# Kernel optimization log

Measured on AMD Instinct MI355X. Metric: run time of the kernel, lower is better.

Reference implementation:

```python
import jax, jax.numpy as jnp
import numpy as np

HEAD = 4
EPS = 1e-12


def _l2norm(x, axis):
    # torch F.normalize: x / max(||x||_2, eps)
    return x / jnp.maximum(jnp.linalg.norm(x, axis=axis, keepdims=True), EPS)


def setup_inputs() -> dict:
    key = jax.random.key(0)
    ks = jax.random.split(key, 12)
    n, t, c, h, w = 2, 7, 96, 96, 96
    inp = {
        "curr_feat": jax.random.normal(ks[0], (n, c, h, w), jnp.float32),
        "index_feat_set_s1": jax.random.normal(ks[1], (n, t, c, h, w), jnp.float32),
        "anchor_feat": jax.random.normal(ks[2], (n, c, h, w), jnp.float32),
        "sparse_feat_set_s1": jax.random.normal(ks[3], (n, t, c, h, w), jnp.float32),
        "sparse_feat_set_s2": jax.random.normal(ks[4], (n, t, c, h, w), jnp.float32),
        "sparse_feat_set_s3": jax.random.normal(ks[5], (n, t, c, h, w), jnp.float32),
        # absolute pixel coordinates (x,y interleaved per frame), mostly in-bounds
        # with a little overshoot to exercise zeros padding of grid_sample
        "location_feat": jax.random.uniform(ks[6], (n, t * 2, h, w), jnp.float32, minval=-2.0, maxval=float(w) + 1.0),
        "proj_w": 0.02 * jax.random.normal(ks[7], (c, c), jnp.float32),
        "proj_b": jnp.zeros((c,), jnp.float32),
        "fusion_w": 0.02 * jax.random.normal(ks[8], (c, 3 * c), jnp.float32),
        "fusion_b": jnp.zeros((c,), jnp.float32),
    }
    return inp


def reference(curr_feat, index_feat_set_s1, anchor_feat, sparse_feat_set_s1,
              sparse_feat_set_s2, sparse_feat_set_s3, location_feat,
              proj_w, proj_b, fusion_w, fusion_b):
    n, c, h, w = anchor_feat.shape
    t = sparse_feat_set_s1.shape[1]
    hd = c // HEAD
    hw = h * w

    # ---- flow-guided nearest grid_sample (align_corners=True, zeros pad) ----
    loc = location_feat.reshape(n, t, 2, h, w)  # (n,t,2,h,w): [x, y] pixel coords
    gx = 2.0 * loc[:, :, 0] / max(w - 1, 1) - 1.0
    gy = 2.0 * loc[:, :, 1] / max(h - 1, 1) - 1.0
    ix = jnp.round((gx + 1.0) * 0.5 * (w - 1))  # nearest (round-half-even, as torch)
    iy = jnp.round((gy + 1.0) * 0.5 * (h - 1))
    valid = (ix >= 0) & (ix <= w - 1) & (iy >= 0) & (iy <= h - 1)
    lin = (jnp.clip(iy, 0, h - 1).astype(jnp.int32) * w
           + jnp.clip(ix, 0, w - 1).astype(jnp.int32)).reshape(n, t, 1, hw)
    vmask = valid.reshape(n, t, 1, hw)

    def sample(f):  # f: (n,t,c,h,w) -> gathered (n,t,c,hw)
        g = jnp.take_along_axis(f.reshape(n, t, c, hw), lin, axis=3)
        return jnp.where(vmask, g, 0.0)

    samp1 = sample(sparse_feat_set_s1)
    samp2 = sample(sparse_feat_set_s2)
    samp3 = sample(sparse_feat_set_s3)
    sampi = sample(index_feat_set_s1)

    # ---- per-pixel multi-head max-correlation over t frames ----
    # queries: normalize over full channel dim c BEFORE splitting into heads
    q = _l2norm(curr_feat.reshape(n, c, hw).transpose(0, 2, 1), -1).reshape(n, hw, HEAD, hd)
    k = _l2norm(sampi.transpose(0, 3, 1, 2), -1).reshape(n, hw, t, HEAD, hd)
    scores = jnp.einsum('npthd,nphd->npht', k, q)  # scale == 1.0 in mode='max'
    corr_soft = jnp.max(scores, axis=3)     # (n,hw,head)
    corr_index = jnp.argmax(scores, axis=3)  # (n,hw,head), first-max like torch

    soft_img = jnp.broadcast_to(corr_soft[..., None], (n, hw, HEAD, hd)) \
                  .reshape(n, h, w, c).transpose(0, 3, 1, 2)  # (n,c,h,w)
    idx = jnp.broadcast_to(corr_index[..., None], (n, hw, HEAD, hd)) \
             .reshape(n, hw, c).transpose(0, 2, 1)[:, None]  # (n,1,c,hw)

    def pick(samp):  # select winning frame per (channel-group, pixel)
        return jnp.take_along_axis(samp, idx, axis=1)[:, 0].reshape(n, c, h, w)

    cat = jnp.concatenate([pick(samp1), pick(samp2), pick(samp3)], axis=1)  # (n,3c,h,w)
    out = jnp.einsum('ndhw,cd->nchw', cat, fusion_w) + fusion_b[None, :, None, None]
    out = out * soft_img
    out = jnp.einsum('nchw,dc->ndhw', out, proj_w) + proj_b[None, :, None, None]
    return out + anchor_feat
```

## Files before the change

### kernel.cpp

```cpp
#include <hip/hip_runtime.h>
#include <hip/hip_bf16.h>

#define N_    2
#define T_    7
#define C_    96
#define H_    96
#define W_    96
#define HW_   9216
#define HEAD_ 4
#define HD_   24
#define C3_   288
#define P_    16
#define QP_   100
#define CATP_ 292
#define NBLK_ (N_ * (HW_ / P_))
#define PLANES_ 14
#define CHUNK_  64
#define NCHUNK_ 144

typedef unsigned int u32;

__device__ __forceinline__ float bits2f(u32 b) {
    union { u32 u; float f; } x; x.u = b; return x.f;
}

__device__ __forceinline__ unsigned short f2bf(float f) {
    union { __hip_bfloat16 h; unsigned short s; } u;
    u.h = __float2bfloat16(f);
    return u.s;
}

template<bool BF16>
__device__ __forceinline__ float ld1(const void* p, int i) {
    if constexpr (BF16) return bits2f(((u32)((const unsigned short*)p)[i]) << 16);
    else                return ((const float*)p)[i];
}

template<bool BF16>
__device__ __forceinline__ void ld4w(const void* p, int i, float w[4]) {
    if constexpr (BF16) {
        const uint2 u = ((const uint2*)p)[i >> 2];
        w[0] = bits2f(u.x << 16);
        w[1] = bits2f(u.x & 0xFFFF0000u);
        w[2] = bits2f(u.y << 16);
        w[3] = bits2f(u.y & 0xFFFF0000u);
    } else {
        const float4 v = *((const float4*)((const float*)p + i));
        w[0] = v.x; w[1] = v.y; w[2] = v.z; w[3] = v.w;
    }
}

template<bool BF16>
__device__ __forceinline__ void st4w(void* p, int i, const float v[4]) {
    if constexpr (BF16) {
        uint2 w;
        w.x = (u32)f2bf(v[0]) | ((u32)f2bf(v[1]) << 16);
        w.y = (u32)f2bf(v[2]) | ((u32)f2bf(v[3]) << 16);
        ((uint2*)p)[i >> 2] = w;
    } else {
        *((float4*)((float*)p + i)) = make_float4(v[0], v[1], v[2], v[3]);
    }
}

__device__ __forceinline__ bool block_detect_bf16(const u32* __restrict__ w,
                                                  int tid, int* s_flag) {
    if (tid < 64) {
        u32 x = w[tid];
        u32 f = x & 0x7FFFu;
        int inwin = (f >= 0x3A00u) && (f <= 0x4200u);
        unsigned long long m = __ballot(inwin);
        if (tid == 0) *s_flag = (__popcll(m) >= 40) ? 1 : 0;
    }
    __syncthreads();
    return *s_flag != 0;
}

template<bool BF16>
__device__ __forceinline__ void transp_body(const void* __restrict__ src,
                                            void* __restrict__ dst,
                                            int bx, int tid, char* tileraw) {
    const int pl = bx / NCHUNK_;
    const int x0 = (bx - pl * NCHUNK_) * CHUNK_;
    if constexpr (BF16) {
        unsigned short (*tile)[CHUNK_ + 2] = (unsigned short (*)[CHUNK_ + 2])tileraw;
        const unsigned short* s = (const unsigned short*)src;
        unsigned short* d = (unsigned short*)dst;
        for (int i = tid; i < C_ * (CHUNK_ / 4); i += 256) {
            int ch = i >> 4, xq = i & 15;
            const ushort4 v = *((const ushort4*)(s + (pl * C_ + ch) * HW_ + x0 + 4 * xq));
            tile[ch][4 * xq + 0] = v.x; tile[ch][4 * xq + 1] = v.y;
            tile[ch][4 * xq + 2] = v.z; tile[ch][4 * xq + 3] = v.w;
        }
        __syncthreads();
        for (int i = tid; i < CHUNK_ * (C_ / 4); i += 256) {
            int p = i / 24, cq = i - p * 24;
            ushort4 v;
            v.x = tile[4 * cq + 0][p]; v.y = tile[4 * cq + 1][p];
            v.z = tile[4 * cq + 2][p]; v.w = tile[4 * cq + 3][p];
            *((ushort4*)(d + (pl * HW_ + x0 + p) * C_ + 4 * cq)) = v;
        }
    } else {
        float (*tile)[CHUNK_ + 1] = (float (*)[CHUNK_ + 1])tileraw;
        const float* s = (const float*)src;
        float* d = (float*)dst;
        for (int i = tid; i < C_ * (CHUNK_ / 4); i += 256) {
            int ch = i >> 4, xq = i & 15;
            const float4 v = *((const float4*)(s + (pl * C_ + ch) * HW_ + x0 + 4 * xq));
            tile[ch][4 * xq + 0] = v.x; tile[ch][4 * xq + 1] = v.y;
            tile[ch][4 * xq + 2] = v.z; tile[ch][4 * xq + 3] = v.w;
        }
        __syncthreads();
        for (int i = tid; i < CHUNK_ * (C_ / 4); i += 256) {
            int p = i / 24, cq = i - p * 24;
            float4 v;
            v.x = tile[4 * cq + 0][p]; v.y = tile[4 * cq + 1][p];
            v.z = tile[4 * cq + 2][p]; v.w = tile[4 * cq + 3][p];
            *((float4*)(d + (pl * HW_ + x0 + p) * C_ + 4 * cq)) = v;
        }
    }
}

__global__ __launch_bounds__(256) void transp_kernel(
    const void* __restrict__ idxf, void* __restrict__ dst,
    const u32* __restrict__ detect_src)
{
    __shared__ __align__(16) char tileraw[C_ * (CHUNK_ + 1) * 4];
    __shared__ int s_flag;
    const int tid = threadIdx.x;
    const bool bf = block_detect_bf16(detect_src, tid, &s_flag);
    if (bf) transp_body<true >(idxf, dst, blockIdx.x, tid, tileraw);
    else    transp_body<false>(idxf, dst, blockIdx.x, tid, tileraw);
}

template<bool BF16, int MODE>
__device__ __forceinline__ void traj_body(
    const void* __restrict__ curr, const void* __restrict__ idxf,
    const void* __restrict__ anchor, const void* __restrict__ s1,
    const void* __restrict__ s2, const void* __restrict__ s3,
    const void* __restrict__ loc, const void* __restrict__ pw,
    const void* __restrict__ pb, const void* __restrict__ fw,
    const void* __restrict__ fb, void* __restrict__ outp,
    const void* __restrict__ kT,
    float* s_u, float (*s_mid)[QP_], int (*s_lin)[P_], float (*s_red)[8],
    float (*s_best)[HEAD_], int (*s_bidx)[HEAD_], float* s_inv)
{
#define S_Q(pp, ch)  s_u[(pp) * QP_ + (ch)]
#define S_K(pp, ch)  s_u[P_ * QP_ + (pp) * QP_ + (ch)]
#define S_CAT(pp, d) s_u[(pp) * CATP_ + (d)]

    const int tid = threadIdx.x;
    const int b  = blockIdx.x;
    const int nn = b / (HW_ / P_);
    const int p0 = (b - nn * (HW_ / P_)) * P_;

    if (tid < T_ * P_) {
        int t = tid / P_, pp = tid - t * P_;
        int p = p0 + pp;
        float x = ld1<BF16>(loc, (nn * 2 * T_ + 2 * t    ) * HW_ + p);
        float y = ld1<BF16>(loc, (nn * 2 * T_ + 2 * t + 1) * HW_ + p);
        float gx = 2.0f * x / 95.0f - 1.0f;
        float gy = 2.0f * y / 95.0f - 1.0f;
        float fx = (gx + 1.0f) * 0.5f * 95.0f;
        float fy = (gy + 1.0f) * 0.5f * 95.0f;
        float ix = rintf(fx), iy = rintf(fy);
        bool v = (ix >= 0.0f) && (ix <= 95.0f) && (iy >= 0.0f) && (iy <= 95.0f);
        s_lin[t][pp] = v ? ((int)iy * W_ + (int)ix) : -1;
    }
    if (tid >= 128 && tid < 128 + P_ * HEAD_) {
        int q = tid - 128;
        s_best[q >> 2][q & 3] = -3.0e38f; s_bidx[q >> 2][q & 3] = 0;
    }

    for (int i = tid; i < C_ * (P_ / 4); i += 256) {
        int ch = i >> 2, pq = i & 3;
        float w[4];
        ld4w<BF16>(curr, (nn * C_ + ch) * HW_ + p0 + 4 * pq, w);
        S_Q(4 * pq + 0, ch) = w[0]; S_Q(4 * pq + 1, ch) = w[1];
        S_Q(4 * pq + 2, ch) = w[2]; S_Q(4 * pq + 3, ch) = w[3];
    }
    __syncthreads();

    if (tid < P_ * 8) {
        int pp = tid >> 3, j = tid & 7;
        float s = 0.f;
        #pragma unroll
        for (int k = 0; k < 12; ++k) { float v = S_Q(pp, j * 12 + k); s += v * v; }
        s_red[pp][j] = s;
    }
    __syncthreads();
    if (tid < P_) {
        float s = 0.f;
        #pragma unroll
        for (int j = 0; j < 8; ++j) s += s_red[tid][j];
        s_inv[tid] = 1.0f / fmaxf(sqrtf(s), 1e-12f);
    }
    __syncthreads();
    for (int i = tid; i < C_ * P_; i += 256) {
        int pp = i & (P_ - 1), ch = i >> 4;
        S_Q(pp, ch) *= s_inv[pp];
    }

    for (int t = 0; t < T_; ++t) {
        __syncthreads();
        if constexpr (MODE >= 1) {
            for (int i = tid; i < 24 * P_; i += 256) {
                int pp = i / 24, j = i - pp * 24;
                int lin = s_lin[t][pp];
                float w[4] = {0.f, 0.f, 0.f, 0.f};
                if (lin >= 0) ld4w<BF16>(kT, ((nn * T_ + t) * HW_ + lin) * C_ + 4 * j, w);
                *((float4*)&S_K(pp, 4 * j)) = make_float4(w[0], w[1], w[2], w[3]);
            }
        } else {
            for (int i = tid; i < C_ * P_; i += 256) {
                int ch = i / P_, pp = i - ch * P_;
                int lin = s_lin[t][pp];
                S_K(pp, ch) = (lin >= 0) ? ld1<BF16>(idxf, ((nn * T_ + t) * C_ + ch) * HW_ + lin) : 0.0f;
            }
        }
        __syncthreads();
        if (tid < P_ * 8) {
            int pp = tid >> 3, j = tid & 7;
            float s = 0.f;
            #pragma unroll
            for (int k = 0; k < 12; ++k) { float v = S_K(pp, j * 12 + k); s += v * v; }
            s_red[pp][j] = s;
        }
        __syncthreads();
        if (tid < P_) {
            float s = 0.f;
            #pragma unroll
            for (int j = 0; j < 8; ++j) s += s_red[tid][j];
            s_inv[tid] = 1.0f / fmaxf(sqrtf(s), 1e-12f);
        }
        __syncthreads();
        if (tid < P_ * HEAD_) {
            int pp = tid >> 2, h = tid & 3;
            float s = 0.f;
            #pragma unroll
            for (int dq = 0; dq < 6; ++dq) {
                const float4 kv = *((const float4*)&S_K(pp, h * HD_ + 4 * dq));
                const float4 qv = *((const float4*)&S_Q(pp, h * HD_ + 4 * dq));
                s += kv.x * qv.x; s += kv.y * qv.y; s += kv.z * qv.z; s += kv.w * qv.w;
            }
            s *= s_inv[pp];
            if (s > s_best[pp][h]) { s_best[pp][h] = s; s_bidx[pp][h] = t; }
        }
    }
    __syncthreads();

    for (int i = tid; i < C3_ * P_; i += 256) {
        int pp = i / C3_, d = i - pp * C3_;
        int set = d / C_, ch = d - set * C_;
        int h = ch / HD_;
        int bt = s_bidx[pp][h];
        int lin = s_lin[bt][pp];
        float v = 0.f;
        if (lin >= 0) {
            const void* sp = (set == 0) ? s1 : (set == 1) ? s2 : s3;
            v = ld1<BF16>(sp, ((nn * T_ + bt) * C_ + ch) * HW_ + lin);
        }
        S_CAT(pp, d) = v;
    }
    __syncthreads();

    if (tid < 96) {
        const int cq = tid >> 2, pq = tid & 3;
        const int co0 = cq * 4, px0 = pq * 4;
        float acc[4][4];
        #pragma unroll
        for (int r = 0; r < 4; ++r)
            #pragma unroll
            for (int k = 0; k < 4; ++k) acc[r][k] = 0.f;
        for (int d = 0; d < C3_; d += 4) {
            float4 cv[4];
            #pragma unroll
            for (int k = 0; k < 4; ++k) cv[k] = *((const float4*)&S_CAT(px0 + k, d));
            #pragma unroll
            for (int r = 0; r < 4; ++r) {
                float w[4]; ld4w<BF16>(fw, (co0 + r) * C3_ + d, w);
                #pragma unroll
                for (int k = 0; k < 4; ++k)
                    acc[r][k] += w[0] * cv[k].x + w[1] * cv[k].y + w[2] * cv[k].z + w[3] * cv[k].w;
            }
        }
        const int hh = co0 / HD_;
        #pragma unroll
        for (int r = 0; r < 4; ++r) {
            float fbv = ld1<BF16>(fb, co0 + r);
            #pragma unroll
            for (int k = 0; k < 4; ++k)
                s_mid[px0 + k][co0 + r] = (acc[r][k] + fbv) * s_best[px0 + k][hh];
        }
    }
    __syncthreads();

    if (tid < 96) {
        const int dq = tid >> 2, pq = tid & 3;
        const int do0 = dq * 4, px0 = pq * 4;
        float acc[4][4];
        #pragma unroll
        for (int r = 0; r < 4; ++r)
            #pragma unroll
            for (int k = 0; k < 4; ++k) acc[r][k] = 0.f;
        for (int c = 0; c < C_; c += 4) {
            float4 mv[4];
            #pragma unroll
            for (int k = 0; k < 4; ++k) mv[k] = *((const float4*)&s_mid[px0 + k][c]);
            #pragma unroll
            for (int r = 0; r < 4; ++r) {
                float w[4]; ld4w<BF16>(pw, (do0 + r) * C_ + c, w);
                #pragma unroll
                for (int k = 0; k < 4; ++k)
                    acc[r][k] += w[0] * mv[k].x + w[1] * mv[k].y + w[2] * mv[k].z + w[3] * mv[k].w;
            }
        }
        #pragma unroll
        for (int r = 0; r < 4; ++r) {
            float pbv = ld1<BF16>(pb, do0 + r);
            float av[4];
            ld4w<BF16>(anchor, (nn * C_ + do0 + r) * HW_ + p0 + px0, av);
            float res[4];
            #pragma unroll
            for (int k = 0; k < 4; ++k) res[k] = acc[r][k] + pbv + av[k];
            st4w<BF16>(outp, (nn * C_ + do0 + r) * HW_ + p0 + px0, res);
        }
    }
#undef S_Q
#undef S_K
#undef S_CAT
}

template<int MODE>
__global__ __launch_bounds__(256) void traj_main(
    const void* __restrict__ curr, const void* __restrict__ idxf,
    const void* __restrict__ anchor, const void* __restrict__ s1,
    const void* __restrict__ s2, const void* __restrict__ s3,
    const void* __restrict__ loc, const void* __restrict__ pw,
    const void* __restrict__ pb, const void* __restrict__ fw,
    const void* __restrict__ fb, void* __restrict__ outp,
    const void* __restrict__ kT)
{
    __shared__ __align__(16) float s_u[P_ * CATP_];
    __shared__ __align__(16) float s_mid[P_][QP_];
    __shared__ int   s_lin[T_][P_];
    __shared__ float s_red[P_][8];
    __shared__ float s_best[P_][HEAD_];
    __shared__ int   s_bidx[P_][HEAD_];
    __shared__ float s_inv[P_];
    __shared__ int   s_flag;

    const bool bf = block_detect_bf16((const u32*)curr, threadIdx.x, &s_flag);
    if (bf) traj_body<true,  MODE>(curr, idxf, anchor, s1, s2, s3, loc, pw, pb, fw, fb,
                                   outp, kT, s_u, s_mid, s_lin, s_red, s_best, s_bidx, s_inv);
    else    traj_body<false, MODE>(curr, idxf, anchor, s1, s2, s3, loc, pw, pb, fw, fb,
                                   outp, kT, s_u, s_mid, s_lin, s_red, s_best, s_bidx, s_inv);
}

extern "C" void kernel_launch(void* const* d_in, const int* in_sizes, int n_in,
                              void* d_out, int out_size, void* d_ws, size_t ws_size,
                              hipStream_t stream) {
    (void)in_sizes; (void)n_in; (void)out_size;
    const unsigned long long SZB = (unsigned long long)N_ * T_ * HW_ * C_ * 4ull;
    void* kT = d_ws;
    const int mode = (ws_size >= SZB) ? 1 : 0;

    dim3 grid(NBLK_), block(256);
    if (mode == 1) {
        transp_kernel<<<dim3(PLANES_ * NCHUNK_), 256, 0, stream>>>(d_in[1], kT, (const u32*)d_in[0]);
        traj_main<1><<<grid, block, 0, stream>>>(d_in[0], d_in[1], d_in[2], d_in[3], d_in[4],
                                                 d_in[5], d_in[6], d_in[7], d_in[8], d_in[9],
                                                 d_in[10], d_out, kT);
    } else {
        traj_main<0><<<grid, block, 0, stream>>>(d_in[0], d_in[1], d_in[2], d_in[3], d_in[4],
                                                 d_in[5], d_in[6], d_in[7], d_in[8], d_in[9],
                                                 d_in[10], d_out, kT);
    }
}
```

Measured before the change: 332.9 us.

## Split fused trajectory kernel into argmax and gather-GEMV kernels

The fused per-block kernel is divided into an argmax kernel, which writes the best score and a gather base offset per pixel and head to workspace, and a second kernel that gathers the winning frames and runs both small projections. Each kernel needs less shared memory and carries its own launch-bounds occupancy hint, and the GEMV stage now uses 192 threads with a 2x4 tile instead of 96 threads with 4x4. The cost is an extra launch plus a small workspace round trip, and the split path now needs a slightly larger workspace before it is chosen.

```diff
diff --git a/kernel.cpp b/kernel.cpp
--- a/kernel.cpp
+++ b/kernel.cpp
@@ -51,6 +51,12 @@
 }
 
 template<bool BF16>
+__device__ __forceinline__ void st1(void* p, int i, float v) {
+    if constexpr (BF16) ((unsigned short*)p)[i] = f2bf(v);
+    else                ((float*)p)[i] = v;
+}
+
+template<bool BF16>
 __device__ __forceinline__ void st4w(void* p, int i, const float v[4]) {
     if constexpr (BF16) {
         uint2 w;
@@ -132,22 +138,16 @@
     else    transp_body<false>(idxf, dst, blockIdx.x, tid, tileraw);
 }
 
-template<bool BF16, int MODE>
-__device__ __forceinline__ void traj_body(
-    const void* __restrict__ curr, const void* __restrict__ idxf,
-    const void* __restrict__ anchor, const void* __restrict__ s1,
-    const void* __restrict__ s2, const void* __restrict__ s3,
-    const void* __restrict__ loc, const void* __restrict__ pw,
-    const void* __restrict__ pb, const void* __restrict__ fw,
-    const void* __restrict__ fb, void* __restrict__ outp,
+template<bool BF16>
+__device__ __forceinline__ void argmax_body(
+    const void* __restrict__ curr, const void* __restrict__ loc,
     const void* __restrict__ kT,
-    float* s_u, float (*s_mid)[QP_], int (*s_lin)[P_], float (*s_red)[8],
+    float* __restrict__ ws_best, int* __restrict__ ws_gbase,
+    float* s_u, int (*s_lin)[P_], float (*s_red)[8],
     float (*s_best)[HEAD_], int (*s_bidx)[HEAD_], float* s_inv)
 {
 #define S_Q(pp, ch)  s_u[(pp) * QP_ + (ch)]
 #define S_K(pp, ch)  s_u[P_ * QP_ + (pp) * QP_ + (ch)]
-#define S_CAT(pp, d) s_u[(pp) * CATP_ + (d)]
-
     const int tid = threadIdx.x;
     const int b  = blockIdx.x;
     const int nn = b / (HW_ / P_);
@@ -202,20 +202,12 @@
 
     for (int t = 0; t < T_; ++t) {
         __syncthreads();
-        if constexpr (MODE >= 1) {
-            for (int i = tid; i < 24 * P_; i += 256) {
-                int pp = i / 24, j = i - pp * 24;
-                int lin = s_lin[t][pp];
-                float w[4] = {0.f, 0.f, 0.f, 0.f};
-                if (lin >= 0) ld4w<BF16>(kT, ((nn * T_ + t) * HW_ + lin) * C_ + 4 * j, w);
-                *((float4*)&S_K(pp, 4 * j)) = make_float4(w[0], w[1], w[2], w[3]);
-            }
-        } else {
-            for (int i = tid; i < C_ * P_; i += 256) {
-                int ch = i / P_, pp = i - ch * P_;
-                int lin = s_lin[t][pp];
-                S_K(pp, ch) = (lin >= 0) ? ld1<BF16>(idxf, ((nn * T_ + t) * C_ + ch) * HW_ + lin) : 0.0f;
-            }
+        for (int i = tid; i < 24 * P_; i += 256) {
+            int pp = i / 24, j = i - pp * 24;
+            int lin = s_lin[t][pp];
+            float w[4] = {0.f, 0.f, 0.f, 0.f};
+            if (lin >= 0) ld4w<BF16>(kT, ((nn * T_ + t) * HW_ + lin) * C_ + 4 * j, w);
+            *((float4*)&S_K(pp, 4 * j)) = make_float4(w[0], w[1], w[2], w[3]);
         }
         __syncthreads();
         if (tid < P_ * 8) {
@@ -246,8 +238,257 @@
             if (s > s_best[pp][h]) { s_best[pp][h] = s; s_bidx[pp][h] = t; }
         }
     }
-    __syncthreads();
-
+    if (tid < P_ * HEAD_) {
+        int pp = tid >> 2, h = tid & 3;
+        int bt = s_bidx[pp][h];
+        int lin = s_lin[bt][pp];
+        int g = (nn * HW_ + p0 + pp) * HEAD_ + h;
+        ws_best[g]  = s_best[pp][h];
+        ws_gbase[g] = (lin >= 0) ? ((nn * T_ + bt) * C_ * HW_ + lin) : -1;
+    }
+#undef S_Q
+#undef S_K
+}
+
+__global__ __launch_bounds__(256, 8) void argmax_kernel(
+    const void* __restrict__ curr, const void* __restrict__ loc,
+    const void* __restrict__ kT,
+    float* __restrict__ ws_best, int* __restrict__ ws_gbase)
+{
+    __shared__ __align__(16) float s_u[2 * P_ * QP_];
+    __shared__ int   s_lin[T_][P_];
+    __shared__ float s_red[P_][8];
+    __shared__ float s_best[P_][HEAD_];
+    __shared__ int   s_bidx[P_][HEAD_];
+    __shared__ float s_inv[P_];
+    __shared__ int   s_flag;
+    const bool bf = block_detect_bf16((const u32*)curr, threadIdx.x, &s_flag);
+    if (bf) argmax_body<true >(curr, loc, kT, ws_best, ws_gbase, s_u, s_lin, s_red, s_best, s_bidx, s_inv);
+    else    argmax_body<false>(curr, loc, kT, ws_best, ws_gbase, s_u, s_lin, s_red, s_best, s_bidx, s_inv);
+}
+
+template<bool BF16>
+__device__ __forceinline__ void catgemv_body(
+    const void* __restrict__ anchor, const void* __restrict__ s1,
+    const void* __restrict__ s2, const void* __restrict__ s3,
+    const void* __restrict__ pw, const void* __restrict__ pb,
+    const void* __restrict__ fw, const void* __restrict__ fb,
+    void* __restrict__ outp,
+    const float* __restrict__ ws_best, const int* __restrict__ ws_gbase,
+    float* s_u, float (*s_mid)[QP_], float (*s_best)[HEAD_], int (*s_gbase)[HEAD_])
+{
+#define S_CAT(pp, d) s_u[(pp) * CATP_ + (d)]
+    const int tid = threadIdx.x;
+    const int b  = blockIdx.x;
+    const int nn = b / (HW_ / P_);
+    const int p0 = (b - nn * (HW_ / P_)) * P_;
+
+    if (tid < P_ * HEAD_) {
+        int pp = tid >> 2, h = tid & 3;
+        int g = (nn * HW_ + p0 + pp) * HEAD_ + h;
+        s_best[pp][h]  = ws_best[g];
+        s_gbase[pp][h] = ws_gbase[g];
+    }
+    __syncthreads();
+
+    for (int i = tid; i < C3_ * P_; i += 256) {
+        int pp = i / C3_, d = i - pp * C3_;
+        int set = d / C_, ch = d - set * C_;
+        int gb = s_gbase[pp][ch / HD_];
+        float v = 0.f;
+        if (gb >= 0) {
+            const void* sp = (set == 0) ? s1 : (set == 1) ? s2 : s3;
+            v = ld1<BF16>(sp, gb + ch * HW_);
+        }
+        S_CAT(pp, d) = v;
+    }
+    __syncthreads();
+
+    if (tid < 192) {
+        const int cp = tid >> 2, pq = tid & 3;
+        const int co0 = cp * 2, px0 = pq * 4;
+        float acc[2][4];
+        #pragma unroll
+        for (int r = 0; r < 2; ++r)
+            #pragma unroll
+            for (int k = 0; k < 4; ++k) acc[r][k] = 0.f;
+        for (int d = 0; d < C3_; d += 4) {
+            float4 cv[4];
+            #pragma unroll
+            for (int k = 0; k < 4; ++k) cv[k] = *((const float4*)&S_CAT(px0 + k, d));
+            #pragma unroll
+            for (int r = 0; r < 2; ++r) {
+                float w[4]; ld4w<BF16>(fw, (co0 + r) * C3_ + d, w);
+                #pragma unroll
+                for (int k = 0; k < 4; ++k)
+                    acc[r][k] += w[0] * cv[k].x + w[1] * cv[k].y + w[2] * cv[k].z + w[3] * cv[k].w;
+            }
+        }
+        const int hh = co0 / HD_;
+        #pragma unroll
+        for (int r = 0; r < 2; ++r) {
+            float fbv = ld1<BF16>(fb, co0 + r);
+            #pragma unroll
+            for (int k = 0; k < 4; ++k)
+                s_mid[px0 + k][co0 + r] = (acc[r][k] + fbv) * s_best[px0 + k][hh];
+        }
+    }
+    __syncthreads();
+
+    if (tid < 192) {
+        const int dp = tid >> 2, pq = tid & 3;
+        const int do0 = dp * 2, px0 = pq * 4;
+        float acc[2][4];
+        #pragma unroll
+        for (int r = 0; r < 2; ++r)
+            #pragma unroll
+            for (int k = 0; k < 4; ++k) acc[r][k] = 0.f;
+        for (int c = 0; c < C_; c += 4) {
+            float4 mv[4];
+            #pragma unroll
+            for (int k = 0; k < 4; ++k) mv[k] = *((const float4*)&s_mid[px0 + k][c]);
+            #pragma unroll
+            for (int r = 0; r < 2; ++r) {
+                float w[4]; ld4w<BF16>(pw, (do0 + r) * C_ + c, w);
+                #pragma unroll
+                for (int k = 0; k < 4; ++k)
+                    acc[r][k] += w[0] * mv[k].x + w[1] * mv[k].y + w[2] * mv[k].z + w[3] * mv[k].w;
+            }
+        }
+        #pragma unroll
+        for (int r = 0; r < 2; ++r) {
+            float pbv = ld1<BF16>(pb, do0 + r);
+            float av[4];
+            ld4w<BF16>(anchor, (nn * C_ + do0 + r) * HW_ + p0 + px0, av);
+            float res[4];
+            #pragma unroll
+            for (int k = 0; k < 4; ++k) res[k] = acc[r][k] + pbv + av[k];
+            st4w<BF16>(outp, (nn * C_ + do0 + r) * HW_ + p0 + px0, res);
+        }
+    }
+#undef S_CAT
+}
+
+__global__ __launch_bounds__(256, 6) void catgemv_kernel(
+    const void* __restrict__ curr, const void* __restrict__ anchor,
+    const void* __restrict__ s1, const void* __restrict__ s2,
+    const void* __restrict__ s3, const void* __restrict__ pw,
+    const void* __restrict__ pb, const void* __restrict__ fw,
+    const void* __restrict__ fb, void* __restrict__ outp,
+    const float* __restrict__ ws_best, const int* __restrict__ ws_gbase)
+{
+    __shared__ __align__(16) float s_u[P_ * CATP_];
+    __shared__ __align__(16) float s_mid[P_][QP_];
+    __shared__ float s_best[P_][HEAD_];
+    __shared__ int   s_gbase[P_][HEAD_];
+    __shared__ int   s_flag;
+    const bool bf = block_detect_bf16((const u32*)curr, threadIdx.x, &s_flag);
+    if (bf) catgemv_body<true >(anchor, s1, s2, s3, pw, pb, fw, fb, outp, ws_best, ws_gbase,
+                                s_u, s_mid, s_best, s_gbase);
+    else    catgemv_body<false>(anchor, s1, s2, s3, pw, pb, fw, fb, outp, ws_best, ws_gbase,
+                                s_u, s_mid, s_best, s_gbase);
+}
+
+template<bool BF16>
+__device__ __forceinline__ void mono_body(
+    const void* __restrict__ curr, const void* __restrict__ idxf,
+    const void* __restrict__ anchor, const void* __restrict__ s1,
+    const void* __restrict__ s2, const void* __restrict__ s3,
+    const void* __restrict__ loc, const void* __restrict__ pw,
+    const void* __restrict__ pb, const void* __restrict__ fw,
+    const void* __restrict__ fb, void* __restrict__ outp,
+    float* s_u, float (*s_mid)[QP_], int (*s_lin)[P_], float (*s_red)[8],
+    float (*s_best)[HEAD_], int (*s_bidx)[HEAD_], float* s_inv)
+{
+#define S_Q(pp, ch)  s_u[(pp) * QP_ + (ch)]
+#define S_K(pp, ch)  s_u[P_ * QP_ + (pp) * QP_ + (ch)]
+#define S_CAT(pp, d) s_u[(pp) * CATP_ + (d)]
+    const int tid = threadIdx.x;
+    const int b  = blockIdx.x;
+    const int nn = b / (HW_ / P_);
+    const int p0 = (b - nn * (HW_ / P_)) * P_;
+
+    if (tid < T_ * P_) {
+        int t = tid / P_, pp = tid - t * P_;
+        int p = p0 + pp;
+        float x = ld1<BF16>(loc, (nn * 2 * T_ + 2 * t    ) * HW_ + p);
+        float y = ld1<BF16>(loc, (nn * 2 * T_ + 2 * t + 1) * HW_ + p);
+        float gx = 2.0f * x / 95.0f - 1.0f;
+        float gy = 2.0f * y / 95.0f - 1.0f;
+        float fx = (gx + 1.0f) * 0.5f * 95.0f;
+        float fy = (gy + 1.0f) * 0.5f * 95.0f;
+        float ix = rintf(fx), iy = rintf(fy);
+        bool v = (ix >= 0.0f) && (ix <= 95.0f) && (iy >= 0.0f) && (iy <= 95.0f);
+        s_lin[t][pp] = v ? ((int)iy * W_ + (int)ix) : -1;
+    }
+    if (tid >= 128 && tid < 128 + P_ * HEAD_) {
+        int q = tid - 128;
+        s_best[q >> 2][q & 3] = -3.0e38f; s_bidx[q >> 2][q & 3] = 0;
+    }
+    for (int i = tid; i < C_ * (P_ / 4); i += 256) {
+        int ch = i >> 2, pq = i & 3;
+        float w[4];
+        ld4w<BF16>(curr, (nn * C_ + ch) * HW_ + p0 + 4 * pq, w);
+        S_Q(4 * pq + 0, ch) = w[0]; S_Q(4 * pq + 1, ch) = w[1];
+        S_Q(4 * pq + 2, ch) = w[2]; S_Q(4 * pq + 3, ch) = w[3];
+    }
+    __syncthreads();
+    if (tid < P_ * 8) {
+        int pp = tid >> 3, j = tid & 7;
+        float s = 0.f;
+        #pragma unroll
+        for (int k = 0; k < 12; ++k) { float v = S_Q(pp, j * 12 + k); s += v * v; }
+        s_red[pp][j] = s;
+    }
+    __syncthreads();
+    if (tid < P_) {
+        float s = 0.f;
+        #pragma unroll
+        for (int j = 0; j < 8; ++j) s += s_red[tid][j];
+        s_inv[tid] = 1.0f / fmaxf(sqrtf(s), 1e-12f);
+    }
+    __syncthreads();
+    for (int i = tid; i < C_ * P_; i += 256) {
+        int pp = i & (P_ - 1), ch = i >> 4;
+        S_Q(pp, ch) *= s_inv[pp];
+    }
+    for (int t = 0; t < T_; ++t) {
+        __syncthreads();
+        for (int i = tid; i < C_ * P_; i += 256) {
+            int ch = i / P_, pp = i - ch * P_;
+            int lin = s_lin[t][pp];
+            S_K(pp, ch) = (lin >= 0) ? ld1<BF16>(idxf, ((nn * T_ + t) * C_ + ch) * HW_ + lin) : 0.0f;
+        }
+        __syncthreads();
+        if (tid < P_ * 8) {
+            int pp = tid >> 3, j = tid & 7;
+            float s = 0.f;
+            #pragma unroll
+            for (int k = 0; k < 12; ++k) { float v = S_K(pp, j * 12 + k); s += v * v; }
+            s_red[pp][j] = s;
+        }
+        __syncthreads();
+        if (tid < P_) {
+            float s = 0.f;
+            #pragma unroll
+            for (int j = 0; j < 8; ++j) s += s_red[tid][j];
+            s_inv[tid] = 1.0f / fmaxf(sqrtf(s), 1e-12f);
+        }
+        __syncthreads();
+        if (tid < P_ * HEAD_) {
+            int pp = tid >> 2, h = tid & 3;
+            float s = 0.f;
+            #pragma unroll
+            for (int dq = 0; dq < 6; ++dq) {
+                const float4 kv = *((const float4*)&S_K(pp, h * HD_ + 4 * dq));
+                const float4 qv = *((const float4*)&S_Q(pp, h * HD_ + 4 * dq));
+                s += kv.x * qv.x; s += kv.y * qv.y; s += kv.z * qv.z; s += kv.w * qv.w;
+            }
+            s *= s_inv[pp];
+            if (s > s_best[pp][h]) { s_best[pp][h] = s; s_bidx[pp][h] = t; }
+        }
+    }
+    __syncthreads();
     for (int i = tid; i < C3_ * P_; i += 256) {
         int pp = i / C3_, d = i - pp * C3_;
         int set = d / C_, ch = d - set * C_;
@@ -262,7 +503,6 @@
         S_CAT(pp, d) = v;
     }
     __syncthreads();
-
     if (tid < 96) {
         const int cq = tid >> 2, pq = tid & 3;
         const int co0 = cq * 4, px0 = pq * 4;
@@ -293,7 +533,6 @@
         }
     }
     __syncthreads();
-
     if (tid < 96) {
         const int dq = tid >> 2, pq = tid & 3;
         const int do0 = dq * 4, px0 = pq * 4;
@@ -330,15 +569,13 @@
 #undef S_CAT
 }
 
-template<int MODE>
-__global__ __launch_bounds__(256) void traj_main(
+__global__ __launch_bounds__(256) void mono_kernel(
     const void* __restrict__ curr, const void* __restrict__ idxf,
     const void* __restrict__ anchor, const void* __restrict__ s1,
     const void* __restrict__ s2, const void* __restrict__ s3,
     const void* __restrict__ loc, const void* __restrict__ pw,
     const void* __restrict__ pb, const void* __restrict__ fw,
-    const void* __restrict__ fb, void* __restrict__ outp,
-    const void* __restrict__ kT)
+    const void* __restrict__ fb, void* __restrict__ outp)
 {
     __shared__ __align__(16) float s_u[P_ * CATP_];
     __shared__ __align__(16) float s_mid[P_][QP_];
@@ -348,31 +585,34 @@
     __shared__ int   s_bidx[P_][HEAD_];
     __shared__ float s_inv[P_];
     __shared__ int   s_flag;
-
     const bool bf = block_detect_bf16((const u32*)curr, threadIdx.x, &s_flag);
-    if (bf) traj_body<true,  MODE>(curr, idxf, anchor, s1, s2, s3, loc, pw, pb, fw, fb,
-                                   outp, kT, s_u, s_mid, s_lin, s_red, s_best, s_bidx, s_inv);
-    else    traj_body<false, MODE>(curr, idxf, anchor, s1, s2, s3, loc, pw, pb, fw, fb,
-                                   outp, kT, s_u, s_mid, s_lin, s_red, s_best, s_bidx, s_inv);
+    if (bf) mono_body<true >(curr, idxf, anchor, s1, s2, s3, loc, pw, pb, fw, fb, outp,
+                             s_u, s_mid, s_lin, s_red, s_best, s_bidx, s_inv);
+    else    mono_body<false>(curr, idxf, anchor, s1, s2, s3, loc, pw, pb, fw, fb, outp,
+                             s_u, s_mid, s_lin, s_red, s_best, s_bidx, s_inv);
 }
 
 extern "C" void kernel_launch(void* const* d_in, const int* in_sizes, int n_in,
                               void* d_out, int out_size, void* d_ws, size_t ws_size,
                               hipStream_t stream) {
     (void)in_sizes; (void)n_in; (void)out_size;
-    const unsigned long long SZB = (unsigned long long)N_ * T_ * HW_ * C_ * 4ull;
-    void* kT = d_ws;
-    const int mode = (ws_size >= SZB) ? 1 : 0;
+    const unsigned long long SZB  = (unsigned long long)N_ * T_ * HW_ * C_ * 4ull;
+    const unsigned long long AUXB = (unsigned long long)N_ * HW_ * HEAD_ * 4ull;
+    char* wsb = (char*)d_ws;
+    void*  kT       = wsb;
+    float* ws_best  = (float*)(wsb + SZB);
+    int*   ws_gbase = (int*)  (wsb + SZB + AUXB);
 
     dim3 grid(NBLK_), block(256);
-    if (mode == 1) {
+    if (ws_size >= SZB + 2 * AUXB) {
         transp_kernel<<<dim3(PLANES_ * NCHUNK_), 256, 0, stream>>>(d_in[1], kT, (const u32*)d_in[0]);
-        traj_main<1><<<grid, block, 0, stream>>>(d_in[0], d_in[1], d_in[2], d_in[3], d_in[4],
-                                                 d_in[5], d_in[6], d_in[7], d_in[8], d_in[9],
-                                                 d_in[10], d_out, kT);
+        argmax_kernel<<<grid, block, 0, stream>>>(d_in[0], d_in[6], kT, ws_best, ws_gbase);
+        catgemv_kernel<<<grid, block, 0, stream>>>(d_in[0], d_in[2], d_in[3], d_in[4], d_in[5],
+                                                   d_in[7], d_in[8], d_in[9], d_in[10], d_out,
+                                                   ws_best, ws_gbase);
     } else {
-        traj_main<0><<<grid, block, 0, stream>>>(d_in[0], d_in[1], d_in[2], d_in[3], d_in[4],
-                                                 d_in[5], d_in[6], d_in[7], d_in[8], d_in[9],
-                                                 d_in[10], d_out, kT);
-    }
-}
+        mono_kernel<<<grid, block, 0, stream>>>(d_in[0], d_in[1], d_in[2], d_in[3], d_in[4],
+                                                d_in[5], d_in[6], d_in[7], d_in[8], d_in[9],
+                                                d_in[10], d_out);
+    }
+}
```

Measured after the change: 323.6 us. -2.8%, faster.
